# Optimization experiments

Hardware: AMD Instinct MI355X
Metric: run time of the kernel (lower is better)

## Reference

```python
import jax, jax.numpy as jnp
import numpy as np
import math

B, H, T, D = 4, 16, 577, 1024   # CLIP ViT-L/336: 576 patches + CLS
NEED = 192                      # need_token_num
GROUP = NEED // 4               # 48 PCA components


def setup_inputs():
    key = jax.random.key(0)
    k1, k2 = jax.random.split(key)
    hidden_states = jax.random.normal(k1, (B, T, D), dtype=jnp.float32)
    attn = jax.random.uniform(k2, (B, H, T, T), dtype=jnp.float32)
    attn_weights = attn / attn.sum(-1, keepdims=True)  # row-stochastic attention
    return {"hidden_states": hidden_states, "attn_weights": attn_weights}


def batch_pca(hidden, q):
    # torch.pca_lowrank(sigmoid(h).transpose(2,1)[:,:,1:], q): center columns, top-q right singular vectors
    M = jax.nn.sigmoid(hidden.astype(jnp.float32)).transpose(0, 2, 1)[:, :, 1:]  # [B, D, N]
    Mc = M - M.mean(axis=1, keepdims=True)
    _, _, Vh = jnp.linalg.svd(Mc, full_matrices=False)      # [B, min(D,N), N]
    V = jnp.abs(jnp.transpose(Vh[:, :q, :], (0, 2, 1)))     # [B, N, q]
    belong = jnp.argmax(V, axis=-1)                          # [B, N]
    return V, belong


def batch_similarity_nms(group_sim, scores, threshold):
    # group_sim [B,G,N,N], scores [B,N,G], threshold [B]
    Bn, G, N, _ = group_sim.shape
    bi = jnp.arange(Bn)[:, None]
    gi = jnp.arange(G)[None, :]

    def cond(state):
        return state[0].sum() > 0

    def body(state):
        ns, rs, counts, gs = state
        max_values = ns.max(axis=1)          # [B,G]
        max_idx = jnp.argmax(ns, axis=1)     # [B,G]
        valid = max_values > 0
        sim_row = group_sim[bi, gi, max_idx]  # [B,G,N] row of selected token
        idx_n = jnp.where(valid, max_idx, N)  # sentinel -> dropped
        rs = rs.at[bi, idx_n, gi].set(gs, mode='drop')
        ns = ns.at[bi, idx_n, gi].set(0.0, mode='drop')
        suppress = sim_row > threshold[:, None, None]          # [B,G,N]
        ns = jnp.where(jnp.transpose(suppress, (0, 2, 1)), 0.0, ns)
        return ns, rs, counts + valid.astype(jnp.int32), gs - 1.0

    init = (scores, scores, jnp.zeros((Bn, G), jnp.int32), jnp.float32(1000.0))
    _, rs, counts, _ = jax.lax.while_loop(cond, body, init)
    return counts, rs  # kept-per-group counts, return_scores


def _forward(hs, attn):
    Bn, T_, _ = hs.shape
    N = T_ - 1
    need, G = NEED, GROUP
    hsc = jax.lax.stop_gradient(hs)
    attnc = jax.lax.stop_gradient(attn)

    V, belong = batch_pca(hsc, G)
    cls_sum = attnc[:, :, 0, 1:].sum(axis=1)                  # [B,N] cls attention
    onehot = belong[:, :, None] == jnp.arange(G)[None, None, :]  # [B,N,G]
    scores = jnp.where(onehot, cls_sum[:, :, None], 0.0).astype(jnp.float32)

    x = hsc[:, 1:, :]
    normalized = x / jnp.maximum(jnp.linalg.norm(x, axis=-1, keepdims=True), 1e-12)
    similarity = jnp.einsum('bnd,bmd->bnm', normalized, normalized).astype(jnp.float32)
    triu = jnp.triu(jnp.ones((N, N), bool), k=1)
    sim_mean = (similarity * triu).sum((-1, -2)) / triu.sum()  # [B]

    m = belong[:, None, :] == jnp.arange(G)[None, :, None]     # [B,G,N]
    mask4 = m[:, :, :, None] | m[:, :, None, :]                # row-or-col in group
    group_sim = jnp.where(mask4, similarity[:, None, :, :], 0.0)  # [B,G,N,N]

    keep_counts, ret_scores = batch_similarity_nms(group_sim, scores, (need / 32.0) * sim_mean)

    group_counts = onehot.sum(axis=1).astype(jnp.int32)        # [B,G]
    lower = jnp.minimum(1, group_counts)
    upper = jnp.minimum(jnp.minimum(5 * math.ceil(need / 64), group_counts), keep_counts)

    def ub_cond(u):
        return jnp.any(u.sum(-1) < need)

    def ub_body(u):
        deficient = (u.sum(-1) < need).astype(u.dtype)
        return jnp.minimum(u + deficient[:, None], group_counts)

    upper = jax.lax.while_loop(ub_cond, ub_body, upper)

    other = jnp.maximum(need - lower.sum(-1) - 1, 0)           # [B]
    norm_counts = keep_counts.astype(jnp.float32) / keep_counts.sum(-1, keepdims=True).astype(jnp.float32)
    csum = jnp.cumsum(norm_counts, axis=-1)
    od = jnp.round(csum * other[:, None].astype(jnp.float32)).astype(jnp.int32)
    od = od - jnp.concatenate([jnp.zeros((Bn, 1), jnp.int32), od[:, :-1]], axis=-1)
    token_d0 = jnp.minimum(od + lower, upper)
    sort_idx_g = jnp.argsort(-keep_counts, axis=-1)            # groups by kept count, desc
    target = other + lower.sum(-1)                             # == need-1 per batch
    bi1 = jnp.arange(Bn)

    def f_cond(state):
        return jnp.any(state[0].sum(-1) < target)

    def f_body(state):
        d, fg = state
        deficient = d.sum(-1) < target
        gidx = jnp.take_along_axis(sort_idx_g, jnp.minimum(fg, G - 1)[:, None], axis=1)[:, 0]
        fill = jnp.minimum(upper[bi1, gidx] - d[bi1, gidx], target - d.sum(-1))
        d = d.at[bi1, gidx].add(jnp.where(deficient, fill, 0))
        return d, fg + deficient.astype(fg.dtype)

    token_d, _ = jax.lax.while_loop(f_cond, f_body, (token_d0, jnp.zeros((Bn,), jnp.int32)))

    # top token_d[b,g] indices per group by return_scores, concatenated in group order
    sort_idx = jnp.transpose(jnp.argsort(-ret_scores, axis=1), (0, 2, 1)).astype(jnp.int32)  # [B,G,N]
    take = jnp.arange(N)[None, None, :] < token_d[:, :, None]  # [B,G,N]
    flat_take = take.reshape(Bn, G * N)
    flat_idx = sort_idx.reshape(Bn, G * N)
    L = need - 1  # token_d sums exactly to target == need-1
    pos = jnp.cumsum(flat_take, axis=1) - 1
    pos = jnp.where(flat_take, pos, L)
    gathered = jnp.zeros((Bn, L), jnp.int32).at[bi1[:, None], pos].set(flat_idx, mode='drop')
    batch_indices = jnp.concatenate([jnp.zeros((Bn, 1), jnp.int32), gathered + 1], axis=1)  # [B, need]
    out = jnp.take_along_axis(hs, batch_indices[:, :, None], axis=1)  # [B, need, D]
    return out, batch_indices


def reference(hidden_states, attn_weights):
    return _forward(hidden_states, attn_weights)
```

## Files before the change

### kernel.cpp

```cpp
#include <hip/hip_runtime.h>
#include <math.h>

constexpr int B_ = 4, T_ = 577, N_ = 576, D_ = 1024, G_ = 48, H_ = 16;
constexpr int NEED_ = 192, L_ = 191;
constexpr int TRIU_CNT = N_ * (N_ - 1) / 2;
constexpr int NB_ = 8;
constexpr int NBAR_ = 640;

constexpr size_t OF_MSIG = 0;
constexpr size_t OF_SIM  = OF_MSIG + (size_t)B_*N_*D_*4;
constexpr size_t OF_A    = OF_SIM  + (size_t)B_*N_*N_*4;
constexpr size_t OF_MS   = OF_A    + (size_t)B_*N_*N_*8;
constexpr size_t OF_INVN = OF_MS   + (size_t)B_*N_*8;
constexpr size_t OF_CLS  = OF_INVN + (size_t)B_*N_*8;
constexpr size_t OF_DT   = OF_CLS  + (size_t)B_*N_*4;
constexpr size_t OF_ET   = OF_DT   + (size_t)B_*N_*8;
constexpr size_t OF_TAU  = OF_ET   + (size_t)B_*N_*8;
constexpr size_t OF_EVAL = OF_TAU  + (size_t)B_*N_*8;
constexpr size_t OF_Z    = OF_EVAL + (size_t)B_*G_*8;
constexpr size_t OF_PART = OF_Z    + (size_t)B_*G_*N_*8;
constexpr size_t OF_THR  = OF_PART + (size_t)B_*36*8;
constexpr size_t OF_BEL  = OF_THR  + 64;
constexpr size_t OF_BAR  = OF_BEL  + (size_t)B_*N_*4;
constexpr size_t OF_FLG  = OF_BAR  + (size_t)B_*NBAR_*4;
constexpr size_t OF_VB   = OF_FLG  + (size_t)B_*16*4;
constexpr size_t OF_WB   = OF_VB   + (size_t)B_*N_*8;
constexpr size_t OF_SG   = OF_WB   + (size_t)B_*2*N_*8;
constexpr size_t OF_KP   = OF_SG   + (size_t)B_*8*8;
constexpr size_t WS_NEEDED = OF_KP + (size_t)B_*2*16*8;

constexpr size_t OF_PV_ALIAS = OF_MSIG + ((size_t)8 << 20);

__device__ __forceinline__ double blockReduceD(double x, double* red) {
  int lane = threadIdx.x & 63, wv = threadIdx.x >> 6;
  int nw = (blockDim.x + 63) >> 6;
  for (int o = 32; o > 0; o >>= 1) x += __shfl_down(x, o);
  __syncthreads();
  if (lane == 0) red[wv] = x;
  __syncthreads();
  double t = red[0];
  for (int i = 1; i < nw; i++) t += red[i];
  return t;
}

__device__ __forceinline__ void blockReduce4(double& x0, double& x1, double& x2,
                                             double& x3, double* red) {
  int lane = threadIdx.x & 63, wv = threadIdx.x >> 6;
  int nw = (blockDim.x + 63) >> 6;
  for (int o = 32; o > 0; o >>= 1) {
    x0 += __shfl_down(x0, o); x1 += __shfl_down(x1, o);
    x2 += __shfl_down(x2, o); x3 += __shfl_down(x3, o);
  }
  __syncthreads();
  if (lane == 0) { red[wv*4+0]=x0; red[wv*4+1]=x1; red[wv*4+2]=x2; red[wv*4+3]=x3; }
  __syncthreads();
  double t0 = red[0], t1 = red[1], t2 = red[2], t3 = red[3];
  for (int i = 1; i < nw; i++) {
    t0 += red[i*4+0]; t1 += red[i*4+1]; t2 += red[i*4+2]; t3 += red[i*4+3];
  }
  x0 = t0; x1 = t1; x2 = t2; x3 = t3;
}

__device__ __forceinline__ double cload(const double* p) {
  return __hip_atomic_load(p, __ATOMIC_RELAXED, __HIP_MEMORY_SCOPE_AGENT);
}
__device__ __forceinline__ void cstore(double* p, double x) {
  __hip_atomic_store(p, x, __ATOMIC_RELAXED, __HIP_MEMORY_SCOPE_AGENT);
}

__device__ __forceinline__ void gbar(int* bar, int slot, int tid) {
  __syncthreads();
  if (tid == 0) {
    __hip_atomic_fetch_add(&bar[slot], 1, __ATOMIC_RELAXED, __HIP_MEMORY_SCOPE_AGENT);
    while (__hip_atomic_load(&bar[slot], __ATOMIC_ACQUIRE, __HIP_MEMORY_SCOPE_AGENT) < NB_)
      __builtin_amdgcn_s_sleep(2);
  }
  __syncthreads();
  __asm__ volatile("" ::: "memory");
}

__global__ void k_prep(const float* __restrict__ hs, float* __restrict__ msig,
                       double* __restrict__ ms, double* __restrict__ invn,
                       int* __restrict__ bars) {
  __shared__ double red[16];
  if (blockIdx.x == 0) {
    for (int i = threadIdx.x; i < B_ * NBAR_; i += blockDim.x) bars[i] = 0;
  }
  int bn = blockIdx.x; int b = bn / N_, n = bn % N_;
  const float* row = hs + ((size_t)b*T_ + (n+1)) * (size_t)D_;
  float* mrow = msig + (size_t)bn * D_;
  double ssig = 0.0, ssq = 0.0;
  for (int d = threadIdx.x; d < D_; d += blockDim.x) {
    float x = row[d];
    float sg = 1.0f / (1.0f + expf(-x));
    mrow[d] = sg;
    ssig += (double)sg;
    ssq  += (double)x * (double)x;
  }
  double tot_sig = blockReduceD(ssig, red);
  double tot_sq  = blockReduceD(ssq, red);
  if (threadIdx.x == 0) {
    ms[bn] = tot_sig;
    invn[bn] = 1.0 / fmax(sqrt(tot_sq), 1e-12);
  }
}

__global__ void k_cls(const float* __restrict__ attn, float* __restrict__ cls) {
  int idx = blockIdx.x * blockDim.x + threadIdx.x;
  if (idx >= B_ * N_) return;
  int b = idx / N_, n = idx % N_;
  float s = 0.0f;
  for (int h = 0; h < H_; h++)
    s += attn[(((size_t)b*H_ + h) * T_ + 0) * T_ + (1 + n)];
  cls[idx] = s;
}

__global__ void k_gemm(const float* __restrict__ hs, const float* __restrict__ msig,
                       const double* __restrict__ ms, const double* __restrict__ invn,
                       double* __restrict__ Aout, float* __restrict__ sim, int mode) {
  __shared__ float As[32][17], Bs[32][17];
  int b = blockIdx.z;
  int bi0 = blockIdx.y * 32, bj0 = blockIdx.x * 32;
  const float* base = (mode == 0) ? (msig + (size_t)b*N_*D_)
                                  : (hs + ((size_t)b*T_ + 1) * (size_t)D_);
  int tid = threadIdx.x;
  int tx = tid & 15, ty = tid >> 4;
  double a00 = 0, a01 = 0, a10 = 0, a11 = 0;
  for (int k0 = 0; k0 < D_; k0 += 16) {
    int r = tid >> 4, c = tid & 15;
    As[r][c] = base[(size_t)(bi0 + r) * D_ + k0 + c];
    Bs[r][c] = base[(size_t)(bj0 + r) * D_ + k0 + c];
    int e = tid + 256; r = e >> 4; c = e & 15;
    As[r][c] = base[(size_t)(bi0 + r) * D_ + k0 + c];
    Bs[r][c] = base[(size_t)(bj0 + r) * D_ + k0 + c];
    __syncthreads();
#pragma unroll
    for (int kk = 0; kk < 16; kk++) {
      double x0 = As[2*ty][kk],   x1 = As[2*ty+1][kk];
      double y0 = Bs[2*tx][kk],   y1 = Bs[2*tx+1][kk];
      a00 += x0*y0; a01 += x0*y1; a10 += x1*y0; a11 += x1*y1;
    }
    __syncthreads();
  }
  int i0 = bi0 + 2*ty, j0 = bj0 + 2*tx;
  if (mode == 0) {
    const double* msb = ms + (size_t)b*N_;
    double* Ab = Aout + (size_t)b*N_*N_;
    const double inv1024 = 1.0 / 1024.0;
    Ab[(size_t)i0*N_ + j0]         = a00 - msb[i0]*msb[j0]*inv1024;
    Ab[(size_t)i0*N_ + j0+1]       = a01 - msb[i0]*msb[j0+1]*inv1024;
    Ab[(size_t)(i0+1)*N_ + j0]     = a10 - msb[i0+1]*msb[j0]*inv1024;
    Ab[(size_t)(i0+1)*N_ + j0+1]   = a11 - msb[i0+1]*msb[j0+1]*inv1024;
  } else {
    const double* iv = invn + (size_t)b*N_;
    float* sb = sim + (size_t)b*N_*N_;
    sb[(size_t)i0*N_ + j0]       = (float)(a00 * iv[i0]*iv[j0]);
    sb[(size_t)i0*N_ + j0+1]     = (float)(a01 * iv[i0]*iv[j0+1]);
    sb[(size_t)(i0+1)*N_ + j0]   = (float)(a10 * iv[i0+1]*iv[j0]);
    sb[(size_t)(i0+1)*N_ + j0+1] = (float)(a11 * iv[i0+1]*iv[j0+1]);
  }
}

__global__ void k_simsum(const float* __restrict__ sim, double* __restrict__ part) {
  __shared__ double red[4];
  int blk = blockIdx.x; int b = blk / 36, s = blk % 36;
  const float* sb = sim + (size_t)b*N_*N_;
  double p = 0.0;
  for (int i = s*16; i < s*16 + 16; i++) {
    const float* row = sb + (size_t)i*N_;
    for (int j = i + 1 + threadIdx.x; j < N_; j += blockDim.x) p += (double)row[j];
  }
  double t = blockReduceD(p, red);
  if (threadIdx.x == 0) part[blk] = t;
}

__global__ void k_thr(const double* __restrict__ part, float* __restrict__ thrF) {
  int b = threadIdx.x;
  if (b < B_) {
    double s = 0.0;
    for (int i = 0; i < 36; i++) s += part[b*36 + i];
    thrF[b] = 6.0f * (float)(s / (double)TRIU_CNT);
  }
}

__global__ __launch_bounds__(512) void k_tridiag_mb(double* __restrict__ Aall,
    double* __restrict__ dT, double* __restrict__ eT, double* __restrict__ tauT,
    double* __restrict__ pv_all, double* __restrict__ wb_all,
    int* __restrict__ bars) {
  __shared__ double rb[3][N_];
  __shared__ double wwb[2][N_];
  __shared__ double red[32];
  int blk = blockIdx.x;
  int b = blk % B_;
  int t = blk / B_;
  double* A  = Aall + (size_t)b*N_*N_;
  double* dv = dT   + (size_t)b*N_;
  double* ev = eT   + (size_t)b*N_;
  double* tv = tauT + (size_t)b*N_;
  double* pvB = pv_all + (size_t)b*2*N_;
  double* wbB = wb_all + (size_t)b*2*N_;
  int* bar = bars + b*NBAR_;
  int tid = threadIdx.x, lane = tid & 63, wv = tid >> 6;

  double sig;
  {
    double ps = 0.0;
    for (int j = tid; j < N_; j += 512) {
      rb[0][j] = 0.0;
      wwb[1][j] = 0.0;
      double a0 = A[j];
      rb[1][j] = a0;
      rb[2][j] = A[(size_t)N_ + j];
      if (j >= 1) ps += a0 * a0;
    }
    sig = blockReduceD(ps, red);
  }

  for (int k = 0; k < N_ - 2; k++) {
    int rot = k % 3;
    double* vp = rb[rot];
    double* vc = rb[(rot + 1) % 3];
    double* r2 = rb[(rot + 2) % 3];
    double* wp = wwb[(k & 1) ^ 1];
    double* wc = wwb[k & 1];
    double* wbk = wbB + (size_t)(k & 1) * N_;
    double* pvk = pvB + (size_t)(k & 1) * N_;

    double sigma = sig;
    double x0 = vc[k + 1];
    double alpha, tauk;
    if (sigma == 0.0) { alpha = 0.0; tauk = 0.0; }
    else {
      alpha = (x0 >= 0.0) ? -sqrt(sigma) : sqrt(sigma);
      tauk = 1.0 / (sigma - alpha * x0);
    }
    __syncthreads();
    if (tid == 0) {
      vc[k + 1] = x0 - alpha;
      if (t == 0) { dv[k] = vc[k]; ev[k] = alpha; tv[k] = tauk; }
    }
    __syncthreads();
    if ((k % NB_) == t)
      for (int j = k + 1 + tid; j < N_; j += 512) A[(size_t)k * N_ + j] = vc[j];

    int rr = (k + 1) % NB_;
    int rofs = t - rr; if (rofs < 0) rofs += NB_;
    for (int r = (k + 1) + rofs + wv * NB_; r < N_; r += 8 * NB_) {
      double* Ar = A + (size_t)r * N_;
      double vrp = vp[r], wrp = wp[r];
      double pd = 0.0;
      if (r == k + 2) {
        for (int j = k + 1 + lane; j < N_; j += 64) {
          double nv = Ar[j] - vrp * wp[j] - wrp * vp[j];
          Ar[j] = nv;
          pd += nv * vc[j];
          if (j >= k + 2) cstore(&pvk[j], nv);
        }
      } else {
        for (int j = k + 1 + lane; j < N_; j += 64) {
          double nv = Ar[j] - vrp * wp[j] - wrp * vp[j];
          Ar[j] = nv;
          pd += nv * vc[j];
        }
      }
      for (int o = 32; o > 0; o >>= 1) pd += __shfl_down(pd, o);
      if (lane == 0) cstore(&wbk[r], tauk * pd);
    }
    gbar(bar, k, tid);

    int i0 = k + 1 + tid;
    bool s0 = (i0 < N_), s1 = (i0 + 512 < N_);
    double w0 = s0 ? cload(&wbk[i0]) : 0.0;
    double w1 = s1 ? cload(&wbk[i0 + 512]) : 0.0;
    double p0 = (s0 && tid > 0) ? cload(&pvk[i0]) : 0.0;
    double p1 = s1 ? cload(&pvk[i0 + 512]) : 0.0;
    double wr1 = cload(&wbk[k + 1]);
    double wr2 = cload(&wbk[k + 2]);
    double vc0 = s0 ? vc[i0] : 0.0;
    double vc1 = s1 ? vc[i0 + 512] : 0.0;
    double vk1 = vc[k + 1], vk2 = vc[k + 2];
    double r20 = s0 ? r2[i0] : 0.0;
    double r21 = s1 ? r2[i0 + 512] : 0.0;
    double a0v = r20 - vk1 * w0 - wr1 * vc0;
    double a1v = r21 - vk1 * w1 - wr1 * vc1;
    double kd = w0 * vc0 + w1 * vc1;
    double sa2 = 0.0, sav = 0.0, sv2 = 0.0;
    if (s0 && tid > 0) { sa2 += a0v*a0v; sav += a0v*vc0; sv2 += vc0*vc0; }
    if (s1)            { sa2 += a1v*a1v; sav += a1v*vc1; sv2 += vc1*vc1; }
    blockReduce4(kd, sa2, sav, sv2, red);
    double K = 0.5 * tauk * kd;
    double c = 2.0 * K * vk1;
    sig = sa2 + 2.0 * c * sav + c * c * sv2;
    double wk2 = wr2 - K * vk2;
    if (s0) {
      double wcj = w0 - K * vc0;
      wc[i0] = wcj;
      r2[i0] = a0v + c * vc0;
      if (tid > 0) vp[i0] = p0 - vk2 * wcj - wk2 * vc0;
    }
    if (s1) {
      double wcj = w1 - K * vc1;
      wc[i0 + 512] = wcj;
      r2[i0 + 512] = a1v + c * vc1;
      vp[i0 + 512] = p1 - vk2 * wcj - wk2 * vc1;
    }
    __syncthreads();
  }

  if (t == 0 && tid == 0) {
    double* r1f = rb[((N_ - 3) + 2) % 3];
    double* r2f = rb[(N_ - 3) % 3];
    dv[N_-2] = r1f[N_-2];
    ev[N_-2] = r1f[N_-1];
    dv[N_-1] = r2f[N_-1];
    ev[N_-1] = 0.0; tv[N_-2] = 0.0; tv[N_-1] = 0.0;
  }
}

__global__ __launch_bounds__(64) void k_eigvals_ms(const double* __restrict__ dT,
    const double* __restrict__ eT, double* __restrict__ eval) {
  __shared__ double sd[N_], se[N_];
  int blk = blockIdx.x; int b = blk / G_, j = blk % G_;
  for (int i = threadIdx.x; i < N_; i += 64) {
    sd[i] = dT[(size_t)b*N_ + i];
    se[i] = eT[(size_t)b*N_ + i];
  }
  __syncthreads();
  int lane = threadIdx.x;
  double lo = 1e300, hi = -1e300;
  for (int i = lane; i < N_; i += 64) {
    double r = ((i > 0) ? fabs(se[i-1]) : 0.0) + ((i < N_-1) ? fabs(se[i]) : 0.0);
    lo = fmin(lo, sd[i] - r); hi = fmax(hi, sd[i] + r);
  }
  for (int o = 32; o > 0; o >>= 1) {
    lo = fmin(lo, __shfl_xor(lo, o));
    hi = fmax(hi, __shfl_xor(hi, o));
  }
  double span = hi - lo + 1e-30;
  lo -= span * 1e-6; hi += span * 1e-6;
  int target = N_ - 1 - j;
  const double PIV = 1e-280;
  for (int round = 0; round < 11; round++) {
    double width = hi - lo;
    double mid = lo + width * ((double)(lane + 1) / 65.0);
    int cnt = 0;
    double q = sd[0] - mid;
    if (q <= PIV) { cnt++; q = fmin(q, -PIV); }
    for (int i = 1; i < N_; i++) {
      q = (sd[i] - mid) - se[i-1]*se[i-1] / q;
      if (q <= PIV) { cnt++; q = fmin(q, -PIV); }
    }
    unsigned long long mask = __ballot(cnt > target);
    double nlo, nhi;
    if (mask == 0ULL) { nlo = lo + width * (64.0 / 65.0); nhi = hi; }
    else {
      int m = __ffsll(mask) - 1;
      nhi = lo + width * ((double)(m + 1) / 65.0);
      nlo = (m == 0) ? lo : lo + width * ((double)m / 65.0);
    }
    lo = nlo; hi = nhi;
  }
  if (lane == 0) eval[(size_t)b*G_ + j] = 0.5 * (lo + hi);
}

__global__ void k_eigvecs(const double* __restrict__ dT, const double* __restrict__ eT,
    const double* __restrict__ eval,
    double* __restrict__ Ud, double* __restrict__ U1, double* __restrict__ U2,
    double* __restrict__ Um, int* __restrict__ Ufl, double* __restrict__ Yv,
    double* __restrict__ Z) {
  __shared__ double sd[N_], se[N_];
  __shared__ double red0;
  __shared__ int cstart[G_];
  __shared__ double sh_ev[G_];
  int b = blockIdx.x;
  for (int i = threadIdx.x; i < N_; i += blockDim.x) {
    sd[i] = dT[(size_t)b*N_ + i]; se[i] = eT[(size_t)b*N_ + i];
  }
  if (threadIdx.x < G_) sh_ev[threadIdx.x] = eval[(size_t)b*G_ + threadIdx.x];
  __syncthreads();
  int j = threadIdx.x;
  size_t sbase = (size_t)b * N_ * G_;
  double* ud = Ud + sbase; double* u1 = U1 + sbase; double* u2 = U2 + sbase;
  double* um = Um + sbase; int* ufl = Ufl + sbase; double* yv = Yv + sbase;
  if (j < G_) {
    double lam = sh_ev[j];
    double GU = 1e-30 * (1.0 + fabs(lam));
    double ak = sd[0] - lam;
    double bk = se[0];
    for (int k = 0; k < N_ - 1; k++) {
      double sub = se[k];
      double diag1 = sd[k+1] - lam;
      double sup1 = (k < N_ - 2) ? se[k+1] : 0.0;
      double udv, u1v, u2v, umv; int flv;
      if (fabs(ak) >= fabs(sub)) {
        double piv = ak;
        if (fabs(piv) < GU) piv = (piv >= 0.0) ? GU : -GU;
        double ml = sub / piv;
        udv = piv; u1v = bk; u2v = 0.0; umv = ml; flv = 0;
        ak = diag1 - ml * bk; bk = sup1;
      } else {
        double ml = ak / sub;
        udv = sub; u1v = diag1; u2v = sup1; umv = ml; flv = 1;
        ak = bk - ml * diag1; bk = -ml * sup1;
      }
      ud[(size_t)k*G_+j] = udv; u1[(size_t)k*G_+j] = u1v; u2[(size_t)k*G_+j] = u2v;
      um[(size_t)k*G_+j] = umv; ufl[(size_t)k*G_+j] = flv;
    }
    { double piv = ak; if (fabs(piv) < GU) piv = (piv >= 0.0) ? GU : -GU;
      ud[(size_t)(N_-1)*G_+j] = piv; u1[(size_t)(N_-1)*G_+j] = 0.0; u2[(size_t)(N_-1)*G_+j] = 0.0; }
    for (int i = 0; i < N_; i++) {
      unsigned s = (unsigned)(i * 2654435761u) ^ (unsigned)((j + 1) * 40503u) ^ (unsigned)(b * 2246822519u);
      s = s * 1664525u + 1013904223u;
      s ^= s >> 16; s = s * 2246822519u;
      double rv = ((double)(s >> 8) * (1.0 / 16777216.0)) * 2.0 - 1.0;
      if (fabs(rv) < 1e-3) rv = 0.5;
      yv[(size_t)i*G_+j] = rv;
    }
    for (int it = 0; it < 3; it++) {
      if (it) {
        double mx = 0.0;
        for (int i = 0; i < N_; i++) mx = fmax(mx, fabs(yv[(size_t)i*G_+j]));
        double sc = 1.0 / fmax(mx, 1e-300);
        for (int i = 0; i < N_; i++) yv[(size_t)i*G_+j] *= sc;
      }
      for (int k = 0; k < N_ - 1; k++) {
        double yk = yv[(size_t)k*G_+j], yk1 = yv[(size_t)(k+1)*G_+j];
        if (ufl[(size_t)k*G_+j]) { double tt = yk; yk = yk1; yk1 = tt; }
        yk1 -= um[(size_t)k*G_+j] * yk;
        yv[(size_t)k*G_+j] = yk; yv[(size_t)(k+1)*G_+j] = yk1;
      }
      double y1, y2 = 0.0;
      { double tt = yv[(size_t)(N_-1)*G_+j] / ud[(size_t)(N_-1)*G_+j];
        yv[(size_t)(N_-1)*G_+j] = tt; y1 = tt; }
      for (int k = N_ - 2; k >= 0; k--) {
        double tt = yv[(size_t)k*G_+j] - u1[(size_t)k*G_+j]*y1 - u2[(size_t)k*G_+j]*y2;
        tt /= ud[(size_t)k*G_+j];
        yv[(size_t)k*G_+j] = tt;
        y2 = y1; y1 = tt;
      }
    }
    double s2 = 0.0;
    for (int i = 0; i < N_; i++) { double tt = yv[(size_t)i*G_+j]; s2 += tt * tt; }
    double inv = 1.0 / sqrt(fmax(s2, 1e-300));
    double* Zj = Z + ((size_t)b*G_ + j) * N_;
    for (int i = 0; i < N_; i++) Zj[i] = yv[(size_t)i*G_+j] * inv;
  }
  __syncthreads();
  if (threadIdx.x == 0) {
    double tol = 1e-10 * (fabs(sh_ev[0]) + 1.0);
    cstart[0] = 0;
    for (int q = 1; q < G_; q++)
      cstart[q] = ((sh_ev[q-1] - sh_ev[q]) < tol) ? cstart[q-1] : q;
  }
  __syncthreads();
  for (int q = 1; q < G_; q++) {
    if (cstart[q] == q) continue;
    double* Zq = Z + ((size_t)b*G_ + q) * N_;
    for (int p = cstart[q]; p < q; p++) {
      double* Zp = Z + ((size_t)b*G_ + p) * N_;
      double dp = 0.0;
      for (int i = threadIdx.x; i < N_; i += blockDim.x) dp += Zq[i] * Zp[i];
      for (int o = 32; o > 0; o >>= 1) dp += __shfl_down(dp, o);
      if (threadIdx.x == 0) red0 = dp;
      __syncthreads();
      double dd = red0;
      for (int i = threadIdx.x; i < N_; i += blockDim.x) Zq[i] -= dd * Zp[i];
      __syncthreads();
    }
    double s2 = 0.0;
    for (int i = threadIdx.x; i < N_; i += blockDim.x) { double tt = Zq[i]; s2 += tt * tt; }
    for (int o = 32; o > 0; o >>= 1) s2 += __shfl_down(s2, o);
    if (threadIdx.x == 0) red0 = s2;
    __syncthreads();
    double inv = 1.0 / sqrt(fmax(red0, 1e-300));
    for (int i = threadIdx.x; i < N_; i += blockDim.x) Zq[i] *= inv;
    __syncthreads();
  }
}

__global__ __launch_bounds__(64) void k_backxf_mb(const double* __restrict__ Aall,
    const double* __restrict__ tauT, double* __restrict__ Z) {
  int blk = blockIdx.x;
  int b = blk / G_, q = blk % G_;
  const double* A = Aall + (size_t)b*N_*N_;
  const double* tau = tauT + (size_t)b*N_;
  double* Zq = Z + ((size_t)b*G_ + q) * N_;
  int lane = threadIdx.x;
  double z[9];
#pragma unroll
  for (int m = 0; m < 9; m++) z[m] = Zq[lane + 64*m];
  for (int k = N_ - 3; k >= 0; k--) {
    double t = tau[k];
    if (t == 0.0) continue;
    const double* vk = A + (size_t)k*N_;
    double vv[9]; double p = 0.0;
#pragma unroll
    for (int m = 0; m < 9; m++) {
      int i = lane + 64*m;
      double vi = (i > k) ? vk[i] : 0.0;
      vv[m] = vi; p += vi * z[m];
    }
    for (int o = 32; o > 0; o >>= 1) p += __shfl_down(p, o);
    p = __shfl(p, 0);
    double s = t * p;
#pragma unroll
    for (int m = 0; m < 9; m++) z[m] -= s * vv[m];
  }
#pragma unroll
  for (int m = 0; m < 9; m++) Zq[lane + 64*m] = z[m];
}

__global__ void k_belong(const double* __restrict__ Z, int* __restrict__ belong) {
  int idx = blockIdx.x * blockDim.x + threadIdx.x;
  if (idx >= B_ * N_) return;
  int b = idx / N_, n = idx % N_;
  const double* Zb = Z + (size_t)b*G_*N_;
  double best = -1.0; int bi = 0;
  for (int q = 0; q < G_; q++) {
    double av = fabs(Zb[(size_t)q*N_ + n]);
    if (av > best) { best = av; bi = q; }
  }
  belong[idx] = bi;
}

__global__ __launch_bounds__(256) void k_nms(const float* __restrict__ sim,
    const float* __restrict__ cls, const int* __restrict__ belong,
    const float* __restrict__ thrF, float* __restrict__ outF) {
  __shared__ float nsv[N_], rsv[N_];
  __shared__ int bl_s[N_];
  __shared__ int lists[N_];
  __shared__ int off[G_ + 1];
  __shared__ int kc[G_], gc[G_], lowv[G_], upv[G_], tokd[G_], sortg[G_], pre[G_ + 1];
  __shared__ int gathered[L_];
  __shared__ int anyv;
  __shared__ float shthr;
  int b = blockIdx.x, tid = threadIdx.x;
  const float* simb = sim + (size_t)b*N_*N_;
  if (tid == 0) shthr = thrF[b];
  if (tid < G_) gc[tid] = 0;
  __syncthreads();
  for (int i = tid; i < N_; i += 256) {
    int g = belong[b*N_ + i];
    bl_s[i] = g;
    float sc = cls[b*N_ + i];
    nsv[i] = sc; rsv[i] = sc;
    atomicAdd(&gc[g], 1);
  }
  __syncthreads();
  if (tid == 0) {
    off[0] = 0;
    for (int g = 0; g < G_; g++) off[g+1] = off[g] + gc[g];
    for (int g = 0; g < G_; g++) pre[g] = off[g];
    for (int n = 0; n < N_; n++) lists[pre[bl_s[n]]++] = n;
  }
  __syncthreads();
  float thr = shthr;
  float gs = 1000.0f;
  int myc = 0;
  for (int iter = 0; iter < N_ + 8; iter++) {
    if (tid == 0) anyv = 0;
    __syncthreads();
    int m = -1;
    if (tid < G_) {
      float mx = 0.0f;
      for (int a = off[tid]; a < off[tid+1]; a++) {
        int n2 = lists[a];
        float vv = nsv[n2];
        if (vv > mx) { mx = vv; m = n2; }
      }
      if (m >= 0) anyv = 1;
    }
    __syncthreads();
    if (m >= 0) {
      rsv[m] = gs;
      nsv[m] = 0.0f;
      const float* srow = simb + (size_t)m*N_;
      for (int a = off[tid]; a < off[tid+1]; a++) {
        int n2 = lists[a];
        if (nsv[n2] > 0.0f && srow[n2] > thr) nsv[n2] = 0.0f;
      }
      myc++;
    }
    gs -= 1.0f;
    __syncthreads();
    if (!anyv) break;
  }
  if (tid < G_) kc[tid] = myc;
  __syncthreads();
  if (tid == 0) {
    int sumkc = 0; for (int g = 0; g < G_; g++) sumkc += kc[g];
    int sumlow = 0;
    for (int g = 0; g < G_; g++) {
      lowv[g] = (gc[g] < 1) ? gc[g] : 1;
      int u = 15; if (gc[g] < u) u = gc[g]; if (kc[g] < u) u = kc[g];
      upv[g] = u; sumlow += lowv[g];
    }
    int su = 0; for (int g = 0; g < G_; g++) su += upv[g];
    while (su < NEED_) {
      su = 0;
      for (int g = 0; g < G_; g++) { int u = upv[g] + 1; if (u > gc[g]) u = gc[g]; upv[g] = u; su += u; }
    }
    int other = NEED_ - sumlow - 1; if (other < 0) other = 0;
    float s = (float)sumkc;
    float c = 0.0f; int prevR = 0;
    float otherf = (float)other;
    for (int g = 0; g < G_; g++) {
      float nc = (float)kc[g] / s;
      c += nc;
      int R = (int)rintf(c * otherf);
      int od = R - prevR; prevR = R;
      int t0 = od + lowv[g]; if (t0 > upv[g]) t0 = upv[g];
      tokd[g] = t0;
    }
    for (int g = 0; g < G_; g++) sortg[g] = g;
    for (int a = 1; a < G_; a++) {
      int vIdx = sortg[a]; int key = kc[vIdx]; int p2 = a - 1;
      while (p2 >= 0 && kc[sortg[p2]] < key) { sortg[p2+1] = sortg[p2]; p2--; }
      sortg[p2+1] = vIdx;
    }
    int target = other + sumlow;
    int sumd = 0; for (int g = 0; g < G_; g++) sumd += tokd[g];
    int fg = 0;
    while (sumd < target) {
      int gi = sortg[(fg < G_-1) ? fg : (G_-1)];
      int fill = upv[gi] - tokd[gi];
      int rem = target - sumd;
      if (rem < fill) fill = rem;
      tokd[gi] += fill; sumd += fill;
      fg++;
      if (fg > 100000) break;
    }
    pre[0] = 0; for (int g = 0; g < G_; g++) pre[g+1] = pre[g] + tokd[g];
  }
  __syncthreads();
  for (int i = tid; i < L_; i += 256) gathered[i] = 0;
  __syncthreads();
  if (tid < G_) {
    int g = tid;
    int td = tokd[g], base = pre[g];
    for (int t = 0; t < td; t++) {
      float bv = -3e38f; int bn2 = 0;
      for (int a = off[g]; a < off[g+1]; a++) {
        int n2 = lists[a];
        float vv = rsv[n2];
        if (vv > bv) { bv = vv; bn2 = n2; }
      }
      rsv[bn2] = -3e38f;
      int pos = base + t;
      if (pos < L_) gathered[pos] = bn2;
    }
  }
  __syncthreads();
  if (tid < NEED_) {
    float val = (tid == 0) ? 0.0f : (float)(gathered[tid - 1] + 1);
    outF[(size_t)B_*NEED_*D_ + (size_t)b*NEED_ + tid] = val;
  }
}

__global__ void k_gather(const float* __restrict__ hs, float* __restrict__ outF) {
  int blk = blockIdx.x;
  int b = blk / NEED_, i = blk % NEED_;
  int idx = (int)outF[(size_t)B_*NEED_*D_ + (size_t)b*NEED_ + i];
  const float4* src = (const float4*)(hs + ((size_t)b*T_ + idx) * (size_t)D_);
  float4* dst = (float4*)(outF + ((size_t)b*NEED_ + i) * (size_t)D_);
  dst[threadIdx.x] = src[threadIdx.x];
}

extern "C" void kernel_launch(void* const* d_in, const int* in_sizes, int n_in,
                              void* d_out, int out_size, void* d_ws, size_t ws_size,
                              hipStream_t stream) {
  if (ws_size < WS_NEEDED) return;
  const float* hs   = (const float*)d_in[0];
  const float* attn = (const float*)d_in[1];
  float* outF = (float*)d_out;
  char* w = (char*)d_ws;
  float*  msig = (float*)(w + OF_MSIG);
  float*  sim  = (float*)(w + OF_SIM);
  double* A    = (double*)(w + OF_A);
  double* ms   = (double*)(w + OF_MS);
  double* invn = (double*)(w + OF_INVN);
  float*  cls  = (float*)(w + OF_CLS);
  double* dT   = (double*)(w + OF_DT);
  double* eT   = (double*)(w + OF_ET);
  double* tauT = (double*)(w + OF_TAU);
  double* eval = (double*)(w + OF_EVAL);
  double* Z    = (double*)(w + OF_Z);
  double* part = (double*)(w + OF_PART);
  float*  thrF = (float*)(w + OF_THR);
  int*    belong = (int*)(w + OF_BEL);
  int*    bars = (int*)(w + OF_BAR);
  double* wb   = (double*)(w + OF_WB);
  double* pv   = (double*)(w + OF_PV_ALIAS);
  double* Ud = (double*)(w + OF_MSIG);
  double* U1 = Ud + (size_t)B_*N_*G_;
  double* U2 = U1 + (size_t)B_*N_*G_;
  double* Um = U2 + (size_t)B_*N_*G_;
  double* Yv = Um + (size_t)B_*N_*G_;
  int*    Ufl = (int*)(Yv + (size_t)B_*N_*G_);

  k_prep<<<B_*N_, 256, 0, stream>>>(hs, msig, ms, invn, bars);
  k_cls<<<(B_*N_ + 255)/256, 256, 0, stream>>>(attn, cls);
  k_gemm<<<dim3(N_/32, N_/32, B_), 256, 0, stream>>>(hs, msig, ms, invn, A, sim, 0);
  k_gemm<<<dim3(N_/32, N_/32, B_), 256, 0, stream>>>(hs, msig, ms, invn, A, sim, 1);
  k_simsum<<<B_*36, 256, 0, stream>>>(sim, part);
  k_thr<<<1, 64, 0, stream>>>(part, thrF);
  k_tridiag_mb<<<B_*NB_, 512, 0, stream>>>(A, dT, eT, tauT, pv, wb, bars);
  k_eigvals_ms<<<B_*G_, 64, 0, stream>>>(dT, eT, eval);
  k_eigvecs<<<B_, 64, 0, stream>>>(dT, eT, eval, Ud, U1, U2, Um, Ufl, Yv, Z);
  k_backxf_mb<<<B_*G_, 64, 0, stream>>>(A, tauT, Z);
  k_belong<<<(B_*N_ + 255)/256, 256, 0, stream>>>(Z, belong);
  k_nms<<<B_, 256, 0, stream>>>(sim, cls, belong, thrF, outF);
  k_gather<<<B_*NEED_, 256, 0, stream>>>(hs, outF);
}
```

Measured before the change: 8.688 ms.

## Finish Householder tridiagonalization tail in one block with LDS-resident trailing matrix

```diff
diff --git a/kernel.cpp b/kernel.cpp
--- a/kernel.cpp
+++ b/kernel.cpp
@@ -6,6 +6,9 @@
 constexpr int TRIU_CNT = N_ * (N_ - 1) / 2;
 constexpr int NB_ = 8;
 constexpr int NBAR_ = 640;
+constexpr int KT_ = 448;
+constexpr int TLR_ = N_ - KT_ - 1;
+constexpr int TLP_ = 128;
 
 constexpr size_t OF_MSIG = 0;
 constexpr size_t OF_SIM  = OF_MSIG + (size_t)B_*N_*D_*4;
@@ -29,7 +32,8 @@
 constexpr size_t OF_KP   = OF_SG   + (size_t)B_*8*8;
 constexpr size_t WS_NEEDED = OF_KP + (size_t)B_*2*16*8;
 
-constexpr size_t OF_PV_ALIAS = OF_MSIG + ((size_t)8 << 20);
+constexpr size_t OF_TB       = (size_t)5 << 20;
+constexpr size_t OF_PV_ALIAS = (size_t)8 << 20;
 
 __device__ __forceinline__ double blockReduceD(double x, double* red) {
   int lane = threadIdx.x & 63, wv = threadIdx.x >> 6;
@@ -186,10 +190,11 @@
 __global__ __launch_bounds__(512) void k_tridiag_mb(double* __restrict__ Aall,
     double* __restrict__ dT, double* __restrict__ eT, double* __restrict__ tauT,
     double* __restrict__ pv_all, double* __restrict__ wb_all,
-    int* __restrict__ bars) {
+    int* __restrict__ bars, double* __restrict__ TBall) {
   __shared__ double rb[3][N_];
   __shared__ double wwb[2][N_];
   __shared__ double red[32];
+  __shared__ double TL[TLR_][TLP_];
   int blk = blockIdx.x;
   int b = blk % B_;
   int t = blk / B_;
@@ -199,6 +204,7 @@
   double* tv = tauT + (size_t)b*N_;
   double* pvB = pv_all + (size_t)b*2*N_;
   double* wbB = wb_all + (size_t)b*2*N_;
+  double* TBb = TBall + (size_t)b*TLR_*TLP_;
   int* bar = bars + b*NBAR_;
   int tid = threadIdx.x, lane = tid & 63, wv = tid >> 6;
 
@@ -216,7 +222,7 @@
     sig = blockReduceD(ps, red);
   }
 
-  for (int k = 0; k < N_ - 2; k++) {
+  for (int k = 0; k < KT_; k++) {
     int rot = k % 3;
     double* vp = rb[rot];
     double* vc = rb[(rot + 1) % 3];
@@ -307,7 +313,96 @@
     __syncthreads();
   }
 
-  if (t == 0 && tid == 0) {
+  {
+    double* vp = rb[KT_ % 3];
+    double* wp = wwb[(KT_ & 1) ^ 1];
+    int rr = (KT_ + 1) % NB_;
+    int rofs = t - rr; if (rofs < 0) rofs += NB_;
+    for (int r = (KT_ + 1) + rofs + wv * NB_; r < N_; r += 8 * NB_) {
+      const double* Ar = A + (size_t)r * N_;
+      double vrp = vp[r], wrp = wp[r];
+      double* Tr = TBb + (size_t)(r - KT_ - 1) * TLP_;
+      for (int j = KT_ + 1 + lane; j < N_; j += 64) {
+        double nv = Ar[j] - vrp * wp[j] - wrp * vp[j];
+        cstore(&Tr[j - KT_ - 1], nv);
+      }
+    }
+    gbar(bar, KT_, tid);
+    if (t != 0) return;
+  }
+
+  for (int i = tid; i < TLR_ * TLP_; i += 512) {
+    int r = i >> 7, c2 = i & (TLP_ - 1);
+    TL[r][c2] = (c2 < TLR_) ? cload(&TBb[(size_t)r * TLP_ + c2]) : 0.0;
+  }
+  for (int j = tid; j < N_; j += 512) { rb[KT_ % 3][j] = 0.0; wwb[(KT_ & 1) ^ 1][j] = 0.0; }
+  __syncthreads();
+
+  for (int k = KT_; k < N_ - 2; k++) {
+    int rot = k % 3;
+    double* vp = rb[rot];
+    double* vc = rb[(rot + 1) % 3];
+    double* r2v = rb[(rot + 2) % 3];
+    double* wp = wwb[(k & 1) ^ 1];
+    double* wc = wwb[k & 1];
+
+    double sigma = sig;
+    double x0 = vc[k + 1];
+    double alpha, tauk;
+    if (sigma == 0.0) { alpha = 0.0; tauk = 0.0; }
+    else {
+      alpha = (x0 >= 0.0) ? -sqrt(sigma) : sqrt(sigma);
+      tauk = 1.0 / (sigma - alpha * x0);
+    }
+    __syncthreads();
+    if (tid == 0) {
+      vc[k + 1] = x0 - alpha;
+      dv[k] = vc[k]; ev[k] = alpha; tv[k] = tauk;
+    }
+    __syncthreads();
+    for (int j = k + 1 + tid; j < N_; j += 512) A[(size_t)k * N_ + j] = vc[j];
+
+    for (int r = k + 1 + wv; r < N_; r += 8) {
+      double* Tr = TL[r - KT_ - 1] - (KT_ + 1);
+      double vrp = vp[r], wrp = wp[r];
+      double pd = 0.0;
+      for (int j = k + 1 + lane; j < N_; j += 64) {
+        double nv = Tr[j] - vrp * wp[j] - wrp * vp[j];
+        Tr[j] = nv;
+        pd += nv * vc[j];
+      }
+      for (int o = 32; o > 0; o >>= 1) pd += __shfl_down(pd, o);
+      if (lane == 0) wc[r] = tauk * pd;
+    }
+    __syncthreads();
+
+    int i0 = k + 1 + tid;
+    bool s0 = (i0 < N_);
+    double w0 = s0 ? wc[i0] : 0.0;
+    double wr1 = wc[k + 1], wr2 = wc[k + 2];
+    double vc0 = s0 ? vc[i0] : 0.0;
+    double vk1 = vc[k + 1], vk2 = vc[k + 2];
+    double r20 = s0 ? r2v[i0] : 0.0;
+    double p0 = (s0 && tid > 0) ? TL[k + 1 - KT_][i0 - KT_ - 1] : 0.0;
+    double a0v = r20 - vk1 * w0 - wr1 * vc0;
+    double kd = w0 * vc0;
+    double sa2 = 0.0, sav = 0.0, sv2 = 0.0;
+    if (s0 && tid > 0) { sa2 = a0v*a0v; sav = a0v*vc0; sv2 = vc0*vc0; }
+    blockReduce4(kd, sa2, sav, sv2, red);
+    double K = 0.5 * tauk * kd;
+    double c = 2.0 * K * vk1;
+    sig = sa2 + 2.0 * c * sav + c * c * sv2;
+    double wk2 = wr2 - K * vk2;
+    if (s0) {
+      double wcj = w0 - K * vc0;
+      wc[i0] = wcj;
+      r2v[i0] = a0v + c * vc0;
+      if (tid > 0) vp[i0] = p0 - vk2 * wcj - wk2 * vc0;
+    }
+    __syncthreads();
+  }
+
+  if (tid == 0) {
     double* r1f = rb[((N_ - 3) + 2) % 3];
     double* r2f = rb[(N_ - 3) % 3];
     dv[N_-2] = r1f[N_-2];
@@ -464,6 +559,7 @@
       if (threadIdx.x == 0) red0 = dp;
       __syncthreads();
       double dd = red0;
+      for (int i = threadIdx.x; i < blockDim.x ? i < N_ : false; i += blockDim.x) {}
       for (int i = threadIdx.x; i < N_; i += blockDim.x) Zq[i] -= dd * Zp[i];
       __syncthreads();
     }
@@ -690,7 +786,8 @@
   int*    belong = (int*)(w + OF_BEL);
   int*    bars = (int*)(w + OF_BAR);
   double* wb   = (double*)(w + OF_WB);
-  double* pv   = (double*)(w + OF_PV_ALIAS);
+  double* pv   = (double*)(w + OF_MSIG + OF_PV_ALIAS);
+  double* TB   = (double*)(w + OF_MSIG + OF_TB);
   double* Ud = (double*)(w + OF_MSIG);
   double* U1 = Ud + (size_t)B_*N_*G_;
   double* U2 = U1 + (size_t)B_*N_*G_;
@@ -704,7 +801,7 @@
   k_gemm<<<dim3(N_/32, N_/32, B_), 256, 0, stream>>>(hs, msig, ms, invn, A, sim, 1);
   k_simsum<<<B_*36, 256, 0, stream>>>(sim, part);
   k_thr<<<1, 64, 0, stream>>>(part, thrF);
-  k_tridiag_mb<<<B_*NB_, 512, 0, stream>>>(A, dT, eT, tauT, pv, wb, bars);
+  k_tridiag_mb<<<B_*NB_, 512, 0, stream>>>(A, dT, eT, tauT, pv, wb, bars, TB);
   k_eigvals_ms<<<B_*G_, 64, 0, stream>>>(dT, eT, eval);
   k_eigvecs<<<B_, 64, 0, stream>>>(dT, eT, eval, Ud, U1, U2, Um, Ufl, Yv, Z);
   k_backxf_mb<<<B_*G_, 64, 0, stream>>>(A, tauT, Z);
```

Measured after the change: 8.869 ms. 2.1% more time.
